# Optimization experiments

Measured on AMD Instinct MI355X. Metric: run time of the kernel, lower is better.

## Reference

```python
import jax, jax.numpy as jnp
import numpy as np

NEG_INF = -1e10  # finite stand-in for torch NEG_INF; safe under logaddexp
EOS = 1
BLANK = -1  # blank is the last vocab index (self.blank = -1)


def setup_inputs() -> dict:
    key = jax.random.key(0)
    k1, k2, k3 = jax.random.split(key, 3)
    T, V = 1500, 32000
    N, U = 8, 10
    ctc_beam = 2048
    ctc_prob = jax.random.normal(k1, (T, V), dtype=jnp.float32)
    g = jax.random.randint(k2, (N, U), 0, V)
    c = jax.random.randint(k3, (N * ctc_beam,), 0, V)
    return {"ctc_prob": ctc_prob, "g": g, "c": c}


def reference(ctc_prob, g, c):
    # --- constructor math ---
    logp = jax.nn.log_softmax(ctc_prob, axis=-1)  # T x V
    T, V = logp.shape
    N, U = g.shape
    NB = c.shape[0]
    ctc_beam = NB // N
    blank_lp = logp[:, BLANK]                     # T
    gamma_b_g0 = jnp.cumsum(blank_lp)             # T  (running blank logprob)
    # state after repeat_interleave(beam) along batch dim -> T x NB
    gamma_b_g = jnp.broadcast_to(gamma_b_g0[:, None], (T, NB))
    gamma_n_g = jnp.full((T, NB), NEG_INF, jnp.float32)
    ctc_score0 = jnp.zeros((NB,), jnp.float32)    # ctc_score repeated to NB

    # --- forward ---
    lp_c = logp[:, c]                             # T x NB, gathered per candidate
    glen = U - 1                                  # static
    start = max(glen, 1)
    if glen == 0:
        init_n = lp_c[0]
    else:
        init_n = jnp.full((NB,), NEG_INF, jnp.float32)
    init_b = jnp.full((NB,), NEG_INF, jnp.float32)
    score0 = init_n
    repeat = jnp.repeat(g[:, -1], ctc_beam) != c  # NB bool
    neg = jnp.float32(NEG_INF)

    def step(carry, xs):
        n_prev, b_prev, score = carry
        gb_gm1, gn_gm1, lp_c_t, lp_b_t = xs
        term = jnp.where(repeat, gn_gm1, neg)
        phi = jnp.logaddexp(gb_gm1, term)
        n_t = jnp.logaddexp(n_prev, phi) + lp_c_t
        b_t = jnp.logaddexp(b_prev, n_prev) + lp_b_t
        score = jnp.logaddexp(score, phi + lp_c_t)
        return (n_t, b_t, score), None

    xs = (
        gamma_b_g[start - 1:T - 1],                               # gamma_b_g[t-1]
        gamma_n_g[start - 1:T - 1],                               # gamma_n_g[t-1]
        lp_c[start:],                                             # ctc_prob[t, c]
        jnp.broadcast_to(blank_lp[start:, None], (T - start, NB)),  # ctc_prob[t, blank]
    )
    (_, _, score), _ = jax.lax.scan(step, (init_n, init_b, score0), xs)

    is_eos = c == EOS
    gamma_nb_g = jnp.logaddexp(gamma_b_g[-1], gamma_n_g[-1])
    score = jnp.where(is_eos, gamma_nb_g, score)
    delta_score = (score - ctc_score0).reshape(-1, ctc_beam)  # N x ctc_beam
    return delta_score
```

## Files before the change

### kernel.cpp

```cpp
#include <hip/hip_runtime.h>
#include <hip/hip_fp16.h>

#define T_DIM   1500
#define ROW_F   32000
#define TOT_F   48000000L
#define START_T 9
#define NB      16384
#define BLOCK   512
#define CPT     32
#define NPAIR   16
#define ROWS    6
#define NCHUNK  250
#define NEGBIG  -3.0e38f
#define EOS_ID  1
#define LN2     0.69314718055994531f
#define L2E     1.44269504088896341f

#if __has_builtin(__builtin_amdgcn_exp2f)
__device__ __forceinline__ float fexp2(float x) { return __builtin_amdgcn_exp2f(x); }
#else
__device__ __forceinline__ float fexp2(float x) { return __expf(x * LN2); }
#endif
#if __has_builtin(__builtin_amdgcn_logf)
__device__ __forceinline__ float flog2(float x) { return __builtin_amdgcn_logf(x); }
#else
__device__ __forceinline__ float flog2(float x) { return __logf(x) * L2E; }
#endif

#define WG_BARRIER() do { \
  asm volatile("s_waitcnt lgkmcnt(0)" ::: "memory"); \
  __builtin_amdgcn_s_barrier(); \
  asm volatile("" ::: "memory"); \
} while (0)

typedef __attribute__((address_space(1))) void* as1_ptr;
typedef __attribute__((address_space(3))) void* as3_ptr;

__global__ __launch_bounds__(BLOCK, 2)
void ctc_k1(const float* __restrict__ P, const int* __restrict__ cidx,
            float* __restrict__ Lws, float* __restrict__ Sblank)
{
  __shared__ __align__(16) __half Ah[64000];
  __shared__ __align__(16) float  Bs[2][4096];
  __shared__ float red[2][12];
  const int tid = threadIdx.x;
  const int w   = tid >> 6;
  const int l   = tid & 63;
  const int q   = blockIdx.x;
  const int t0  = q * ROWS;

  unsigned cidp[NPAIR];
  float acc[CPT];
#pragma unroll
  for (int j = 0; j < NPAIR; ++j) {
    unsigned c0 = (unsigned)cidx[(2*j  )*BLOCK + tid] * 2u;
    unsigned c1 = (unsigned)cidx[(2*j+1)*BLOCK + tid] * 2u;
    cidp[j] = c0 | (c1 << 16);
    acc[2*j] = 0.f; acc[2*j+1] = 0.f;
  }

  float blankv  = 0.f;
  float Blocal2 = 0.f;

  auto ISSUE = [&](int g) {
    const int rr = g >> 3, ss = g & 7;
    long f0 = (long)(t0 + rr) * ROW_F + (ss << 12) + (w << 9) + (l << 2);
    long f1 = f0 + 256;
    f0 = (f0 > TOT_F - 4) ? (TOT_F - 4) : f0;
    f1 = (f1 > TOT_F - 4) ? (TOT_F - 4) : f1;
    float* b0 = &Bs[g & 1][(w << 9)];
    __builtin_amdgcn_global_load_lds((as1_ptr)(P + f0), (as3_ptr)(b0      ), 16, 0, 0);
    __builtin_amdgcn_global_load_lds((as1_ptr)(P + f1), (as3_ptr)(b0 + 256), 16, 0, 0);
  };

  auto STAGE_ROW = [&](int gbase, int nb, bool LASTROW) {
    float psum = 0.f;
#pragma unroll
    for (int ss = 0; ss < 8; ++ss) {
      const int g = gbase + ss;
      if (LASTROW && ss == 7) { asm volatile("s_waitcnt vmcnt(0)" ::: "memory"); }
      else                    { asm volatile("s_waitcnt vmcnt(2)" ::: "memory"); }
      const int len = (ss == 7) ? 3328 : 4096;
      const int rem = len - (w << 9);
      const int nj  = (rem >= 512) ? 8 : (rem > 0 ? (rem >> 6) : 0);
      float x[8];
      const float* Bsl = &Bs[g & 1][(w << 9) + l];
#pragma unroll
      for (int j = 0; j < 8; ++j) if (j < nj) x[j] = Bsl[j << 6];
      asm volatile("s_waitcnt lgkmcnt(0)" ::: "memory");
      if (g + 2 < 48) ISSUE(g + 2);
      __half* Adst = Ah + nb * ROW_F + (ss << 12) + (w << 9) + l;
#pragma unroll
      for (int j = 0; j < 8; ++j) if (j < nj) {
        float px = fexp2(x[j] * L2E);
        psum += px;
        Adst[j << 6] = __float2half_rn(px);
        if (ss == 7 && j == 3 && tid == 447) blankv = x[j];
      }
    }
#pragma unroll
    for (int d = 1; d < 64; d <<= 1) psum += __shfl_xor(psum, d);
    if (l == 0) red[nb][w] = psum;
    if (tid == 447) red[nb][8] = blankv * L2E;
  };

  auto GATHER = [&](int r) {
    const int b = r & 1;
    float sum = red[b][0];
#pragma unroll
    for (int ww = 1; ww < 8; ++ww) sum += red[b][ww];
    const float lse2 = flog2(sum);
    if (t0 + r >= START_T) {
      const float sc = fexp2(Blocal2 - lse2);
      const char* rb = (const char*)Ah + b * 64000;
#pragma unroll
      for (int j = 0; j < NPAIR; ++j) {
        unsigned pk = cidp[j];
        float p0 = __half2float(*(const __half*)(rb + (pk & 0xffffu)));
        float p1 = __half2float(*(const __half*)(rb + (pk >> 16)));
        acc[2*j]   = fmaf(sc, p0, acc[2*j]);
        acc[2*j+1] = fmaf(sc, p1, acc[2*j+1]);
      }
    }
    Blocal2 += red[b][8] - lse2;
  };

  ISSUE(0); ISSUE(1);
  STAGE_ROW(0, 0, false);
  WG_BARRIER();

  for (int r = 0; r < 5; ++r) {
    GATHER(r);
    STAGE_ROW((r + 1) * 8, (r + 1) & 1, r == 4);
    WG_BARRIER();
  }
  GATHER(5);

#pragma unroll
  for (int k = 0; k < CPT; ++k) {
    float L = (acc[k] > 0.f) ? flog2(acc[k]) * LN2 : NEGBIG;
    Lws[(long)q*NB + k*BLOCK + tid] = L;
  }
  if (tid == 0) Sblank[q] = Blocal2 * LN2;
}

#define K3_BLOCK 256

__global__ __launch_bounds__(K3_BLOCK)
void ctc_k3(const float* __restrict__ Lws, const float* __restrict__ Sblank,
            const int* __restrict__ cidx, float* __restrict__ out, int nchunk)
{
  __shared__ float base[258];
  __shared__ float wsum[4];
  __shared__ float pm[4][64], pv[4][64];
  const int tid = threadIdx.x;

  float orig = (tid < nchunk) ? Sblank[tid] : 0.f;
  float x = orig;
#pragma unroll
  for (int d = 1; d < 64; d <<= 1) {
    float y = __shfl_up(x, d);
    if ((tid & 63) >= d) x += y;
  }
  if ((tid & 63) == 63) wsum[tid >> 6] = x;
  __syncthreads();
  {
    const int ww = tid >> 6;
    float pre = 0.f;
    if (ww > 0) pre += wsum[0];
    if (ww > 1) pre += wsum[1];
    if (ww > 2) pre += wsum[2];
    x += pre;
  }
  if (tid < nchunk)      base[tid] = x - orig;
  if (tid == nchunk - 1) base[nchunk] = x;
  __syncthreads();

  const int c = tid & 63;
  const int p = tid >> 6;
  const int i = blockIdx.x * 64 + c;
  const int c0 = p * 63;
  int c1 = c0 + 63; if (c1 > nchunk) c1 = nchunk;

  float mm = NEGBIG, ssum = 0.f;
#pragma unroll 8
  for (int q2 = c0; q2 < c1; ++q2) {
    float L = Lws[(long)q2*NB + i] + base[q2];
    float nm = fmaxf(mm, L);
    ssum = ssum*__expf(mm - nm) + __expf(L - nm);
    mm = nm;
  }
  pm[p][c] = mm; pv[p][c] = ssum;
  __syncthreads();
  if (p == 0) {
#pragma unroll
    for (int pp = 1; pp < 4; ++pp) {
      float om = pm[pp][c], os = pv[pp][c];
      float nm = fmaxf(mm, om);
      ssum = ssum*__expf(mm - nm) + os*__expf(om - nm);
      mm = nm;
    }
    float sc = mm + __logf(ssum);
    out[i] = (cidx[i] == EOS_ID) ? base[nchunk] : sc;
  }
}

extern "C" void kernel_launch(void* const* d_in, const int* in_sizes, int n_in,
                              void* d_out, int out_size, void* d_ws, size_t ws_size,
                              hipStream_t stream)
{
  const float* P    = (const float*)d_in[0];
  const int*   cidx = (const int*)d_in[2];
  float*       out  = (float*)d_out;

  float* Lws    = (float*)d_ws;
  float* Sblank = Lws + (long)NCHUNK * NB;

  ctc_k1<<<dim3(NCHUNK), dim3(BLOCK), 0, stream>>>(P, cidx, Lws, Sblank);
  ctc_k3<<<dim3(NB / 64), dim3(K3_BLOCK), 0, stream>>>(Lws, Sblank, cidx, out, NCHUNK);
}
```

Baseline: 56.04 us.

## Split work into 512 chunks with single-buffered LDS for higher occupancy

Stage 1 now processes about 3 rows per block across 512 blocks instead of 6 rows across 250. It keeps only one fp16 probability row in LDS plus a small 16-byte-per-lane float4 staging buffer, and raises launch bounds to 4 blocks per CU. The goal is better CU fill on the 256-CU device and more resident waves to hide load latency. In exchange, each row needs an extra barrier because staging and gather can no longer overlap through double buffering, stage 2 must reduce over 512 partials with a 512-thread block, and the Lws workspace roughly doubles.

```diff
diff --git a/kernel.cpp b/kernel.cpp
--- a/kernel.cpp
+++ b/kernel.cpp
@@ -3,14 +3,12 @@
 
 #define T_DIM   1500
 #define ROW_F   32000
-#define TOT_F   48000000L
 #define START_T 9
 #define NB      16384
 #define BLOCK   512
 #define CPT     32
 #define NPAIR   16
-#define ROWS    6
-#define NCHUNK  250
+#define NCHUNK  512
 #define NEGBIG  -3.0e38f
 #define EOS_ID  1
 #define LN2     0.69314718055994531f
@@ -36,18 +34,24 @@
 typedef __attribute__((address_space(1))) void* as1_ptr;
 typedef __attribute__((address_space(3))) void* as3_ptr;
 
-__global__ __launch_bounds__(BLOCK, 2)
+struct alignas(8) H4p { __half2 a, b; };
+
+__global__ __launch_bounds__(BLOCK, 4)
 void ctc_k1(const float* __restrict__ P, const int* __restrict__ cidx,
             float* __restrict__ Lws, float* __restrict__ Sblank)
 {
-  __shared__ __align__(16) __half Ah[64000];
-  __shared__ __align__(16) float  Bs[2][4096];
-  __shared__ float red[2][12];
+  __shared__ __align__(16) __half A[32000];
+  __shared__ __align__(16) float  B[2][8][256];
+  __shared__ float red[12];
   const int tid = threadIdx.x;
   const int w   = tid >> 6;
   const int l   = tid & 63;
   const int q   = blockIdx.x;
-  const int t0  = q * ROWS;
+  const int t0  = (q * T_DIM) >> 9;
+  const int t1  = ((q + 1) * T_DIM) >> 9;
+  const int rows = t1 - t0;
+
+  const int NW = (w < 5) ? 16 : 15;
 
   unsigned cidp[NPAIR];
   float acc[CPT];
@@ -59,60 +63,52 @@
     acc[2*j] = 0.f; acc[2*j+1] = 0.f;
   }
 
-  float blankv  = 0.f;
+  int ir = 0, ii = 0, isl = 0;
+  int psl = 0;
+  auto ISSUE1 = [&]() {
+    if (ir < rows) {
+      const float* src = P + (long)(t0 + ir) * ROW_F + ((w + (ii << 3)) << 8) + (l << 2);
+      __builtin_amdgcn_global_load_lds((as1_ptr)src, (as3_ptr)&B[isl][w][0], 16, 0, 0);
+      isl ^= 1;
+      if (++ii == NW) { ii = 0; ++ir; }
+    }
+  };
+
   float Blocal2 = 0.f;
 
-  auto ISSUE = [&](int g) {
-    const int rr = g >> 3, ss = g & 7;
-    long f0 = (long)(t0 + rr) * ROW_F + (ss << 12) + (w << 9) + (l << 2);
-    long f1 = f0 + 256;
-    f0 = (f0 > TOT_F - 4) ? (TOT_F - 4) : f0;
-    f1 = (f1 > TOT_F - 4) ? (TOT_F - 4) : f1;
-    float* b0 = &Bs[g & 1][(w << 9)];
-    __builtin_amdgcn_global_load_lds((as1_ptr)(P + f0), (as3_ptr)(b0      ), 16, 0, 0);
-    __builtin_amdgcn_global_load_lds((as1_ptr)(P + f1), (as3_ptr)(b0 + 256), 16, 0, 0);
+  auto STAGE_ROW = [&](int r) {
+    float psum = 0.f;
+    const bool lastrow = (r == rows - 1);
+#pragma unroll 16
+    for (int i = 0; i < 16; ++i) {
+      if (i >= NW) break;
+      if (lastrow && i == NW - 1) { asm volatile("s_waitcnt vmcnt(0)" ::: "memory"); }
+      else                        { asm volatile("s_waitcnt vmcnt(1)" ::: "memory"); }
+      const float4 x = *(const float4*)&B[psl][w][l << 2];
+      asm volatile("s_waitcnt lgkmcnt(0)" ::: "memory");
+      ISSUE1();
+      psl ^= 1;
+      const int g = w + (i << 3);
+      float p0 = fexp2(x.x * L2E), p1 = fexp2(x.y * L2E);
+      float p2 = fexp2(x.z * L2E), p3 = fexp2(x.w * L2E);
+      psum += (p0 + p1) + (p2 + p3);
+      H4p h; h.a = __floats2half2_rn(p0, p1); h.b = __floats2half2_rn(p2, p3);
+      *(H4p*)((char*)A + (g << 9) + (l << 3)) = h;
+      if (g == 124 && l == 63) red[8] = x.w * L2E;
+    }
+#pragma unroll
+    for (int d = 1; d < 64; d <<= 1) psum += __shfl_xor(psum, d);
+    if (l == 0) red[w] = psum;
   };
 
-  auto STAGE_ROW = [&](int gbase, int nb, bool LASTROW) {
-    float psum = 0.f;
-#pragma unroll
-    for (int ss = 0; ss < 8; ++ss) {
-      const int g = gbase + ss;
-      if (LASTROW && ss == 7) { asm volatile("s_waitcnt vmcnt(0)" ::: "memory"); }
-      else                    { asm volatile("s_waitcnt vmcnt(2)" ::: "memory"); }
-      const int len = (ss == 7) ? 3328 : 4096;
-      const int rem = len - (w << 9);
-      const int nj  = (rem >= 512) ? 8 : (rem > 0 ? (rem >> 6) : 0);
-      float x[8];
-      const float* Bsl = &Bs[g & 1][(w << 9) + l];
-#pragma unroll
-      for (int j = 0; j < 8; ++j) if (j < nj) x[j] = Bsl[j << 6];
-      asm volatile("s_waitcnt lgkmcnt(0)" ::: "memory");
-      if (g + 2 < 48) ISSUE(g + 2);
-      __half* Adst = Ah + nb * ROW_F + (ss << 12) + (w << 9) + l;
-#pragma unroll
-      for (int j = 0; j < 8; ++j) if (j < nj) {
-        float px = fexp2(x[j] * L2E);
-        psum += px;
-        Adst[j << 6] = __float2half_rn(px);
-        if (ss == 7 && j == 3 && tid == 447) blankv = x[j];
-      }
-    }
-#pragma unroll
-    for (int d = 1; d < 64; d <<= 1) psum += __shfl_xor(psum, d);
-    if (l == 0) red[nb][w] = psum;
-    if (tid == 447) red[nb][8] = blankv * L2E;
-  };
-
   auto GATHER = [&](int r) {
-    const int b = r & 1;
-    float sum = red[b][0];
-#pragma unroll
-    for (int ww = 1; ww < 8; ++ww) sum += red[b][ww];
+    float sum = red[0];
+#pragma unroll
+    for (int ww = 1; ww < 8; ++ww) sum += red[ww];
     const float lse2 = flog2(sum);
     if (t0 + r >= START_T) {
       const float sc = fexp2(Blocal2 - lse2);
-      const char* rb = (const char*)Ah + b * 64000;
+      const char* rb = (const char*)A;
 #pragma unroll
       for (int j = 0; j < NPAIR; ++j) {
         unsigned pk = cidp[j];
@@ -122,19 +118,17 @@
         acc[2*j+1] = fmaf(sc, p1, acc[2*j+1]);
       }
     }
-    Blocal2 += red[b][8] - lse2;
+    Blocal2 += red[8] - lse2;
   };
 
-  ISSUE(0); ISSUE(1);
-  STAGE_ROW(0, 0, false);
-  WG_BARRIER();
-
-  for (int r = 0; r < 5; ++r) {
+  ISSUE1(); ISSUE1();
+
+  for (int r = 0; r < rows; ++r) {
+    STAGE_ROW(r);
+    WG_BARRIER();
     GATHER(r);
-    STAGE_ROW((r + 1) * 8, (r + 1) & 1, r == 4);
     WG_BARRIER();
   }
-  GATHER(5);
 
 #pragma unroll
   for (int k = 0; k < CPT; ++k) {
@@ -144,15 +138,15 @@
   if (tid == 0) Sblank[q] = Blocal2 * LN2;
 }
 
-#define K3_BLOCK 256
+#define K3_BLOCK 512
 
 __global__ __launch_bounds__(K3_BLOCK)
 void ctc_k3(const float* __restrict__ Lws, const float* __restrict__ Sblank,
             const int* __restrict__ cidx, float* __restrict__ out, int nchunk)
 {
-  __shared__ float base[258];
-  __shared__ float wsum[4];
-  __shared__ float pm[4][64], pv[4][64];
+  __shared__ float base[513];
+  __shared__ float wsum[8];
+  __shared__ float pm[8][64], pv[8][64];
   const int tid = threadIdx.x;
 
   float orig = (tid < nchunk) ? Sblank[tid] : 0.f;
@@ -167,20 +161,18 @@
   {
     const int ww = tid >> 6;
     float pre = 0.f;
-    if (ww > 0) pre += wsum[0];
-    if (ww > 1) pre += wsum[1];
-    if (ww > 2) pre += wsum[2];
+    for (int k = 0; k < ww; ++k) pre += wsum[k];
     x += pre;
   }
-  if (tid < nchunk)      base[tid] = x - orig;
+  base[tid] = x - orig;
   if (tid == nchunk - 1) base[nchunk] = x;
   __syncthreads();
 
   const int c = tid & 63;
   const int p = tid >> 6;
   const int i = blockIdx.x * 64 + c;
-  const int c0 = p * 63;
-  int c1 = c0 + 63; if (c1 > nchunk) c1 = nchunk;
+  const int c0 = p * 64;
+  int c1 = c0 + 64; if (c1 > nchunk) c1 = nchunk;
 
   float mm = NEGBIG, ssum = 0.f;
 #pragma unroll 8
@@ -194,7 +186,7 @@
   __syncthreads();
   if (p == 0) {
 #pragma unroll
-    for (int pp = 1; pp < 4; ++pp) {
+    for (int pp = 1; pp < 8; ++pp) {
       float om = pm[pp][c], os = pv[pp][c];
       float nm = fmaxf(mm, om);
       ssum = ssum*__expf(mm - nm) + os*__expf(om - nm);
```

Measured after the change: 65.16 us. +16.3%, slower.
